# Kernel tuning notes

Hardware: AMD Instinct MI355X
Metric: run time of the kernel (lower is better)

The kernel has to match this reference:

```python
import jax, jax.numpy as jnp
import numpy as np

COMMITMENT_COST = 0.25
NUM_EMBEDDINGS = 4096
EMBEDDING_DIM = 256


def setup_inputs() -> dict:
    key = jax.random.key(0)
    k1, k2 = jax.random.split(key)
    inputs = jax.random.normal(k1, (32, EMBEDDING_DIM, 2048), dtype=jnp.float32)
    # nn.Embedding weight initialized uniform(-1/K, 1/K)
    codebook = jax.random.uniform(
        k2, (NUM_EMBEDDINGS, EMBEDDING_DIM), dtype=jnp.float32,
        minval=-1.0 / NUM_EMBEDDINGS, maxval=1.0 / NUM_EMBEDDINGS)
    return {"inputs": inputs, "codebook": codebook}


def reference(inputs, codebook):
    B, D, S = inputs.shape
    sg = jax.lax.stop_gradient
    # [B, D, S] -> [B*S, D]
    flat = jnp.transpose(inputs, (0, 2, 1)).reshape(-1, D)
    distances = (jnp.sum(flat ** 2, axis=1, keepdims=True)
                 + jnp.sum(codebook ** 2, axis=1)
                 - 2.0 * flat @ codebook.T)
    encoding_indices = jnp.argmin(distances, axis=1)  # [N]
    # direct gather (same math as one-hot @ codebook)
    quantized = codebook[encoding_indices].reshape(B, S, D)
    quantized = jnp.transpose(quantized, (0, 2, 1))  # [B, D, S]
    e_latent_loss = jnp.mean((sg(quantized) - inputs) ** 2)
    q_latent_loss = jnp.mean((quantized - sg(inputs)) ** 2)
    loss = COMMITMENT_COST * e_latent_loss + q_latent_loss
    # straight-through estimator
    quantized_st = inputs + sg(quantized - inputs)
    return quantized_st, loss
```

## Files before the change

### kernel.cpp

```cpp
#include <hip/hip_runtime.h>

#define K_CODES 4096
#define DIM 256
#define SEQ 2048
#define NTOK 65536

typedef __bf16 bf16x8 __attribute__((ext_vector_type(8)));
typedef float floatx4 __attribute__((ext_vector_type(4)));
typedef unsigned short u16x8 __attribute__((ext_vector_type(8)));

__device__ __forceinline__ unsigned short f2bf(float f) {
    union { float f; unsigned int u; } v; v.f = f;
    unsigned int u = v.u;
    unsigned int r = u + 0x7fffu + ((u >> 16) & 1u);
    return (unsigned short)(r >> 16);
}

__device__ __forceinline__ void async_cp16(const void* g, const void* lds_base) {
    typedef __attribute__((address_space(1))) const unsigned int guint;
    typedef __attribute__((address_space(3))) unsigned int luint;
    __builtin_amdgcn_global_load_lds(
        (guint*)(unsigned long long)g,
        (luint*)(unsigned int)(unsigned long long)lds_base,
        16, 0, 0);
}

__global__ __launch_bounds__(256) void k_prep(const float* __restrict__ cb,
        unsigned short* __restrict__ cb_swz, float* __restrict__ norms,
        float* __restrict__ loss_slot) {
    const int c = blockIdx.x;
    const int t = threadIdx.x;
    const int row_loc = t >> 3;
    const int ks = t & 7;
    const int row = c * 32 + row_loc;
    const float* src = cb + (size_t)row * DIM + ks * 32;
    float vals[32];
    float s = 0.0f;
    #pragma unroll
    for (int i = 0; i < 8; ++i) {
        floatx4 v = *(const floatx4*)(src + i * 4);
        #pragma unroll
        for (int j = 0; j < 4; ++j) { vals[i * 4 + j] = v[j]; s += v[j] * v[j]; }
    }
    const int ns = row_loc >> 4, col = row_loc & 15;
    #pragma unroll
    for (int quad = 0; quad < 4; ++quad) {
        u16x8 p;
        #pragma unroll
        for (int j = 0; j < 8; ++j) p[j] = f2bf(vals[quad * 8 + j]);
        *(u16x8*)(cb_swz + ((size_t)((c * 16 + ns * 8 + ks) * 64 + quad * 16 + col)) * 8) = p;
    }
    s += __shfl_xor(s, 1); s += __shfl_xor(s, 2); s += __shfl_xor(s, 4);
    if (ks == 0) norms[row] = s + 0.25f;
    if (c == 0 && t == 0) *loss_slot = 0.0f;
}

__global__ __launch_bounds__(256, 2) void k_argmin(const float* __restrict__ x,
        const unsigned short* __restrict__ cb_swz, const float* __restrict__ norms,
        unsigned int* __restrict__ halfmin, float* __restrict__ loss_slot) {
    __shared__ __align__(16) unsigned short xs[64 * 264];
    __shared__ __align__(16) unsigned short ring[2][8192];
    __shared__ float wpart[4];
    const int t = threadIdx.x;
    const int lane = t & 63, w = t >> 6;
    const int col = lane & 15, quad = lane >> 4;
    const int bx = blockIdx.x;
    const int h = bx & 1;
    const int tb = (bx >> 1) * 256;
    const int b = tb >> 11, s0 = tb & 2047;
    const float* xin = x + (size_t)b * DIM * SEQ;

    {
        const char* src = (const char*)cb_swz + (size_t)h * 64 * 16384;
        #pragma unroll
        for (int i = 0; i < 4; ++i)
            async_cp16(src + i * 4096 + w * 1024 + lane * 16,
                       (char*)ring[0] + i * 4096 + w * 1024);
    }

    bf16x8 af[4][8];
    float a2 = 0.0f;
    const int dg = t >> 4, sq = (t & 15) * 4;
    for (int ph = 0; ph < 4; ++ph) {
        const int sbase = s0 + ph * 64 + sq;
        for (int i = 0; i < 16; ++i) {
            int d = i * 16 + dg;
            floatx4 v = *(const floatx4*)(xin + (size_t)d * SEQ + sbase);
            a2 += v[0]*v[0] + v[1]*v[1] + v[2]*v[2] + v[3]*v[3];
            #pragma unroll
            for (int j = 0; j < 4; ++j) xs[(sq + j) * 264 + d] = f2bf(-2.0f * v[j]);
        }
        __syncthreads();
        if (w == ph) {
            #pragma unroll
            for (int m = 0; m < 4; ++m)
                #pragma unroll
                for (int ks = 0; ks < 8; ++ks)
                    af[m][ks] = *(const bf16x8*)&xs[(m * 16 + col) * 264
                                                    + quad * 8 + ks * 32];
        }
        __syncthreads();
    }
    #pragma unroll
    for (int off = 1; off < 64; off <<= 1) a2 += __shfl_xor(a2, off);
    if (lane == 0) wpart[w] = a2;
    __syncthreads();
    if (t == 0 && h == 0)
        atomicAdd(loss_slot,
                  (wpart[0] + wpart[1] + wpart[2] + wpart[3]) * (1.25f / 16777216.0f));

    unsigned int minkey[4][4];
    #pragma unroll
    for (int m = 0; m < 4; ++m)
        #pragma unroll
        for (int r = 0; r < 4; ++r) minkey[m][r] = 0xFFFFFFFFu;

    #pragma unroll 1
    for (int c = 0; c < 64; ++c) {
        __syncthreads();
        if (c < 63) {
            const char* src = (const char*)cb_swz + (size_t)(h * 64 + c + 1) * 16384;
            char* dst = (char*)ring[(c + 1) & 1];
            #pragma unroll
            for (int i = 0; i < 4; ++i)
                async_cp16(src + i * 4096 + w * 1024 + lane * 16,
                           dst + i * 4096 + w * 1024);
        }
        const unsigned short* buf = ring[c & 1];
        #pragma unroll
        for (int ns = 0; ns < 2; ++ns) {
            const float nv = norms[(h * 64 + c) * 32 + ns * 16 + col];
            bf16x8 bfrag[8];
            #pragma unroll
            for (int ks = 0; ks < 8; ++ks)
                bfrag[ks] = *(const bf16x8*)&buf[((ns * 8 + ks) * 64 + lane) * 8];
            floatx4 acc[4];
            #pragma unroll
            for (int m = 0; m < 4; ++m) acc[m] = (floatx4){nv, nv, nv, nv};
            #pragma unroll
            for (int ks = 0; ks < 8; ++ks)
                #pragma unroll
                for (int m = 0; m < 4; ++m)
                    acc[m] = __builtin_amdgcn_mfma_f32_16x16x32_bf16(
                                 af[m][ks], bfrag[ks], acc[m], 0, 0, 0);
            const unsigned int code = (unsigned int)((h * 64 + c) * 32 + ns * 16 + col);
            #pragma unroll
            for (int m = 0; m < 4; ++m)
                #pragma unroll
                for (int r = 0; r < 4; ++r) {
                    unsigned int key = (__float_as_uint(acc[m][r]) & 0xFFFFF000u) | code;
                    minkey[m][r] = key < minkey[m][r] ? key : minkey[m][r];
                }
        }
    }

    #pragma unroll
    for (int m = 0; m < 4; ++m)
        #pragma unroll
        for (int r = 0; r < 4; ++r) {
            unsigned int k = minkey[m][r];
            #pragma unroll
            for (int off = 8; off >= 1; off >>= 1) {
                unsigned int o = __shfl_xor(k, off);
                k = o < k ? o : k;
            }
            if (col == 0)
                halfmin[h * NTOK + tb + w * 64 + m * 16 + quad * 4 + r] = k;
        }
}

__global__ __launch_bounds__(256) void k_gather(const float* __restrict__ cb,
        const unsigned int* __restrict__ halfmin, float* __restrict__ out,
        float* __restrict__ loss_slot) {
    __shared__ int sidx[128];
    __shared__ float wp2[2];
    const int t = threadIdx.x;
    const int tb = blockIdx.x * 128;
    const int b = tb >> 11, s0 = tb & 2047;
    if (t < 128) {
        unsigned int k0 = halfmin[tb + t], k1 = halfmin[NTOK + tb + t];
        unsigned int km = k0 < k1 ? k0 : k1;
        sidx[t] = (int)(km & 0xFFFu);
        float dv = __uint_as_float(km & 0xFFFFF000u) - 0.25f;
        #pragma unroll
        for (int off = 1; off < 64; off <<= 1) dv += __shfl_xor(dv, off);
        if ((t & 63) == 0) wp2[t >> 6] = dv;
    }
    __syncthreads();
    if (t == 0) atomicAdd(loss_slot, (wp2[0] + wp2[1]) * (1.25f / 16777216.0f));
    const int q = t >> 3, dg = t & 7;
    int rows[4];
    #pragma unroll
    for (int k = 0; k < 4; ++k) rows[k] = sidx[q * 4 + k];
    float* ob = out + (size_t)b * DIM * SEQ + s0 + q * 4;
    #pragma unroll
    for (int i = 0; i < 8; ++i) {
        const int d0 = i * 32 + dg * 4;
        floatx4 v0 = *(const floatx4*)(cb + (size_t)rows[0] * DIM + d0);
        floatx4 v1 = *(const floatx4*)(cb + (size_t)rows[1] * DIM + d0);
        floatx4 v2 = *(const floatx4*)(cb + (size_t)rows[2] * DIM + d0);
        floatx4 v3 = *(const floatx4*)(cb + (size_t)rows[3] * DIM + d0);
        #pragma unroll
        for (int j = 0; j < 4; ++j) {
            floatx4 o = {v0[j], v1[j], v2[j], v3[j]};
            *(floatx4*)(ob + (size_t)(d0 + j) * SEQ) = o;
        }
    }
}

extern "C" void kernel_launch(void* const* d_in, const int* in_sizes, int n_in,
                              void* d_out, int out_size, void* d_ws, size_t ws_size,
                              hipStream_t stream) {
    const float* inputs   = (const float*)d_in[0];
    const float* codebook = (const float*)d_in[1];
    float* out = (float*)d_out;
    unsigned short* cb_swz = (unsigned short*)d_ws;
    float* norms = (float*)((char*)d_ws + (size_t)K_CODES * DIM * 2);
    unsigned int* halfmin = (unsigned int*)((char*)d_ws + (size_t)K_CODES * DIM * 2
                                            + K_CODES * 4);
    float* loss_slot = out + (out_size - 1);

    hipLaunchKernelGGL(k_prep,   dim3(K_CODES / 32),   dim3(256), 0, stream,
                       codebook, cb_swz, norms, loss_slot);
    hipLaunchKernelGGL(k_argmin, dim3(NTOK / 256 * 2), dim3(256), 0, stream,
                       inputs, cb_swz, norms, halfmin, loss_slot);
    hipLaunchKernelGGL(k_gather, dim3(NTOK / 128),     dim3(256), 0, stream,
                       codebook, halfmin, out, loss_slot);
}
```

Baseline: 239.9 us.

## Halve argmin token tile, alias x staging onto ring buffer, raise occupancy

The argmin kernel now handles 128 tokens per block instead of 256, so each wave holds two A-fragment sets instead of four. The separate padded x staging array is removed and its data is staged in the second ring buffer with an XOR swizzle in place of padding, which cuts LDS use. Launch bounds go from 2 to 3 blocks per SIMD and the grid doubles. The aim is more waves in flight to hide latency, at the cost of loading each codebook tile twice as often per token, which raises L2 traffic and lowers MFMA reuse per B fragment.

After: 257.7 us. 7.4% more time.

```diff
diff --git a/kernel.cpp b/kernel.cpp
--- a/kernel.cpp
+++ b/kernel.cpp
@@ -55,18 +55,18 @@
     if (c == 0 && t == 0) *loss_slot = 0.0f;
 }
 
-__global__ __launch_bounds__(256, 2) void k_argmin(const float* __restrict__ x,
+__global__ __launch_bounds__(256, 3) void k_argmin(const float* __restrict__ x,
         const unsigned short* __restrict__ cb_swz, const float* __restrict__ norms,
         unsigned int* __restrict__ halfmin, float* __restrict__ loss_slot) {
-    __shared__ __align__(16) unsigned short xs[64 * 264];
     __shared__ __align__(16) unsigned short ring[2][8192];
     __shared__ float wpart[4];
+    unsigned short* xs = ring[1];
     const int t = threadIdx.x;
     const int lane = t & 63, w = t >> 6;
     const int col = lane & 15, quad = lane >> 4;
     const int bx = blockIdx.x;
     const int h = bx & 1;
-    const int tb = (bx >> 1) * 256;
+    const int tb = (bx >> 1) * 128;
     const int b = tb >> 11, s0 = tb & 2047;
     const float* xin = x + (size_t)b * DIM * SEQ;
 
@@ -78,26 +78,31 @@
                        (char*)ring[0] + i * 4096 + w * 1024);
     }
 
-    bf16x8 af[4][8];
+    bf16x8 af0[8], af1[8];
     float a2 = 0.0f;
-    const int dg = t >> 4, sq = (t & 15) * 4;
-    for (int ph = 0; ph < 4; ++ph) {
-        const int sbase = s0 + ph * 64 + sq;
-        for (int i = 0; i < 16; ++i) {
-            int d = i * 16 + dg;
+    const int q = t & 7, dgp = t >> 3, sq = q * 4;
+    for (int p = 0; p < 4; ++p) {
+        const int sbase = s0 + p * 32 + sq;
+        #pragma unroll
+        for (int i = 0; i < 8; ++i) {
+            const int d = i * 32 + dgp;
             floatx4 v = *(const floatx4*)(xin + (size_t)d * SEQ + sbase);
             a2 += v[0]*v[0] + v[1]*v[1] + v[2]*v[2] + v[3]*v[3];
-            #pragma unroll
-            for (int j = 0; j < 4; ++j) xs[(sq + j) * 264 + d] = f2bf(-2.0f * v[j]);
+            const int chs = (d >> 3) ^ q;
+            #pragma unroll
+            for (int j = 0; j < 4; ++j)
+                xs[(sq + j) * 256 + chs * 8 + (d & 7)] = f2bf(-2.0f * v[j]);
         }
         __syncthreads();
-        if (w == ph) {
-            #pragma unroll
-            for (int m = 0; m < 4; ++m)
-                #pragma unroll
-                for (int ks = 0; ks < 8; ++ks)
-                    af[m][ks] = *(const bf16x8*)&xs[(m * 16 + col) * 264
-                                                    + quad * 8 + ks * 32];
+        if (w == p) {
+            #pragma unroll
+            for (int ks = 0; ks < 8; ++ks)
+                af0[ks] = *(const bf16x8*)
+                    &xs[col * 256 + (((quad + ks * 4) ^ (col >> 2)) * 8)];
+            #pragma unroll
+            for (int ks = 0; ks < 8; ++ks)
+                af1[ks] = *(const bf16x8*)
+                    &xs[(16 + col) * 256 + (((quad + ks * 4) ^ (4 + (col >> 2))) * 8)];
         }
         __syncthreads();
     }
@@ -109,11 +114,9 @@
         atomicAdd(loss_slot,
                   (wpart[0] + wpart[1] + wpart[2] + wpart[3]) * (1.25f / 16777216.0f));
 
-    unsigned int minkey[4][4];
-    #pragma unroll
-    for (int m = 0; m < 4; ++m)
-        #pragma unroll
-        for (int r = 0; r < 4; ++r) minkey[m][r] = 0xFFFFFFFFu;
+    unsigned int minkey0[4], minkey1[4];
+    #pragma unroll
+    for (int r = 0; r < 4; ++r) { minkey0[r] = 0xFFFFFFFFu; minkey1[r] = 0xFFFFFFFFu; }
 
     #pragma unroll 1
     for (int c = 0; c < 64; ++c) {
@@ -134,39 +137,45 @@
             #pragma unroll
             for (int ks = 0; ks < 8; ++ks)
                 bfrag[ks] = *(const bf16x8*)&buf[((ns * 8 + ks) * 64 + lane) * 8];
-            floatx4 acc[4];
-            #pragma unroll
-            for (int m = 0; m < 4; ++m) acc[m] = (floatx4){nv, nv, nv, nv};
-            #pragma unroll
-            for (int ks = 0; ks < 8; ++ks)
-                #pragma unroll
-                for (int m = 0; m < 4; ++m)
-                    acc[m] = __builtin_amdgcn_mfma_f32_16x16x32_bf16(
-                                 af[m][ks], bfrag[ks], acc[m], 0, 0, 0);
+            floatx4 acc0 = (floatx4){nv, nv, nv, nv};
+            floatx4 acc1 = (floatx4){nv, nv, nv, nv};
+            #pragma unroll
+            for (int ks = 0; ks < 8; ++ks) {
+                acc0 = __builtin_amdgcn_mfma_f32_16x16x32_bf16(
+                           af0[ks], bfrag[ks], acc0, 0, 0, 0);
+                acc1 = __builtin_amdgcn_mfma_f32_16x16x32_bf16(
+                           af1[ks], bfrag[ks], acc1, 0, 0, 0);
+            }
             const unsigned int code = (unsigned int)((h * 64 + c) * 32 + ns * 16 + col);
             #pragma unroll
-            for (int m = 0; m < 4; ++m)
-                #pragma unroll
-                for (int r = 0; r < 4; ++r) {
-                    unsigned int key = (__float_as_uint(acc[m][r]) & 0xFFFFF000u) | code;
-                    minkey[m][r] = key < minkey[m][r] ? key : minkey[m][r];
-                }
-        }
-    }
-
-    #pragma unroll
-    for (int m = 0; m < 4; ++m)
-        #pragma unroll
-        for (int r = 0; r < 4; ++r) {
-            unsigned int k = minkey[m][r];
-            #pragma unroll
-            for (int off = 8; off >= 1; off >>= 1) {
-                unsigned int o = __shfl_xor(k, off);
-                k = o < k ? o : k;
+            for (int r = 0; r < 4; ++r) {
+                unsigned int k0 = (__float_as_uint(acc0[r]) & 0xFFFFF000u) | code;
+                minkey0[r] = k0 < minkey0[r] ? k0 : minkey0[r];
+                unsigned int k1 = (__float_as_uint(acc1[r]) & 0xFFFFF000u) | code;
+                minkey1[r] = k1 < minkey1[r] ? k1 : minkey1[r];
             }
-            if (col == 0)
-                halfmin[h * NTOK + tb + w * 64 + m * 16 + quad * 4 + r] = k;
-        }
+        }
+    }
+
+    #pragma unroll
+    for (int r = 0; r < 4; ++r) {
+        unsigned int k = minkey0[r];
+        #pragma unroll
+        for (int off = 8; off >= 1; off >>= 1) {
+            unsigned int o = __shfl_xor(k, off);
+            k = o < k ? o : k;
+        }
+        if (col == 0)
+            halfmin[h * NTOK + tb + w * 32 + quad * 4 + r] = k;
+        unsigned int k2 = minkey1[r];
+        #pragma unroll
+        for (int off = 8; off >= 1; off >>= 1) {
+            unsigned int o = __shfl_xor(k2, off);
+            k2 = o < k2 ? o : k2;
+        }
+        if (col == 0)
+            halfmin[h * NTOK + tb + w * 32 + 16 + quad * 4 + r] = k2;
+    }
 }
 
 __global__ __launch_bounds__(256) void k_gather(const float* __restrict__ cb,
@@ -222,7 +231,7 @@
 
     hipLaunchKernelGGL(k_prep,   dim3(K_CODES / 32),   dim3(256), 0, stream,
                        codebook, cb_swz, norms, loss_slot);
-    hipLaunchKernelGGL(k_argmin, dim3(NTOK / 256 * 2), dim3(256), 0, stream,
+    hipLaunchKernelGGL(k_argmin, dim3(NTOK / 128 * 2), dim3(256), 0, stream,
                        inputs, cb_swz, norms, halfmin, loss_slot);
     hipLaunchKernelGGL(k_gather, dim3(NTOK / 128),     dim3(256), 0, stream,
                        codebook, halfmin, out, loss_slot);
```

## Double codebook chunk per stage, alias x staging into ring buffer with XOR swizzle

Applied to the files above, without the earlier changes.

The codebook pipeline now moves 64 codes (32 KB) per stage instead of 32, which halves the number of barrier-separated iterations. The x staging buffer reuses the second ring slot instead of its own padded array, with an XOR swizzle replacing the padding to avoid LDS bank conflicts. This keeps shared memory about the same while amortising sync and prefetch overhead. The cost is larger per-stage loads and less slack in prefetch timing.

Result: no change. 237.7 us (-0.9%).

```diff
diff --git a/kernel.cpp b/kernel.cpp
--- a/kernel.cpp
+++ b/kernel.cpp
@@ -58,9 +58,10 @@
 __global__ __launch_bounds__(256, 2) void k_argmin(const float* __restrict__ x,
         const unsigned short* __restrict__ cb_swz, const float* __restrict__ norms,
         unsigned int* __restrict__ halfmin, float* __restrict__ loss_slot) {
-    __shared__ __align__(16) unsigned short xs[64 * 264];
-    __shared__ __align__(16) unsigned short ring[2][8192];
+    __shared__ __align__(16) unsigned short ring0[16384];
+    __shared__ __align__(16) unsigned short ring1[16384];
     __shared__ float wpart[4];
+    unsigned short* xs = ring1;
     const int t = threadIdx.x;
     const int lane = t & 63, w = t >> 6;
     const int col = lane & 15, quad = lane >> 4;
@@ -71,33 +72,38 @@
     const float* xin = x + (size_t)b * DIM * SEQ;
 
     {
-        const char* src = (const char*)cb_swz + (size_t)h * 64 * 16384;
-        #pragma unroll
-        for (int i = 0; i < 4; ++i)
+        const char* src = (const char*)cb_swz + (size_t)h * 1048576;
+        #pragma unroll
+        for (int i = 0; i < 8; ++i)
             async_cp16(src + i * 4096 + w * 1024 + lane * 16,
-                       (char*)ring[0] + i * 4096 + w * 1024);
+                       (char*)ring0 + i * 4096 + w * 1024);
     }
 
     bf16x8 af[4][8];
     float a2 = 0.0f;
-    const int dg = t >> 4, sq = (t & 15) * 4;
+    const int dg = t >> 4, sq = (t & 15) * 4, key = t & 7;
     for (int ph = 0; ph < 4; ++ph) {
         const int sbase = s0 + ph * 64 + sq;
+        #pragma unroll
         for (int i = 0; i < 16; ++i) {
-            int d = i * 16 + dg;
+            const int d = i * 16 + dg;
             floatx4 v = *(const floatx4*)(xin + (size_t)d * SEQ + sbase);
             a2 += v[0]*v[0] + v[1]*v[1] + v[2]*v[2] + v[3]*v[3];
-            #pragma unroll
-            for (int j = 0; j < 4; ++j) xs[(sq + j) * 264 + d] = f2bf(-2.0f * v[j]);
+            const int chs = (d >> 3) ^ key;
+            #pragma unroll
+            for (int j = 0; j < 4; ++j)
+                xs[(sq + j) * 256 + chs * 8 + (d & 7)] = f2bf(-2.0f * v[j]);
         }
         __syncthreads();
         if (w == ph) {
             #pragma unroll
-            for (int m = 0; m < 4; ++m)
+            for (int m = 0; m < 4; ++m) {
+                const int rk = (m * 4 + (col >> 2)) & 7;
                 #pragma unroll
                 for (int ks = 0; ks < 8; ++ks)
-                    af[m][ks] = *(const bf16x8*)&xs[(m * 16 + col) * 264
-                                                    + quad * 8 + ks * 32];
+                    af[m][ks] = *(const bf16x8*)
+                        &xs[(m * 16 + col) * 256 + ((quad + ks * 4) ^ rk) * 8];
+            }
         }
         __syncthreads();
     }
@@ -116,20 +122,21 @@
         for (int r = 0; r < 4; ++r) minkey[m][r] = 0xFFFFFFFFu;
 
     #pragma unroll 1
-    for (int c = 0; c < 64; ++c) {
+    for (int cc = 0; cc < 32; ++cc) {
         __syncthreads();
-        if (c < 63) {
-            const char* src = (const char*)cb_swz + (size_t)(h * 64 + c + 1) * 16384;
-            char* dst = (char*)ring[(c + 1) & 1];
-            #pragma unroll
-            for (int i = 0; i < 4; ++i)
+        if (cc < 31) {
+            const char* src = (const char*)cb_swz + (size_t)h * 1048576
+                              + (size_t)(cc + 1) * 32768;
+            char* dst = (char*)(((cc + 1) & 1) ? ring1 : ring0);
+            #pragma unroll
+            for (int i = 0; i < 8; ++i)
                 async_cp16(src + i * 4096 + w * 1024 + lane * 16,
                            dst + i * 4096 + w * 1024);
         }
-        const unsigned short* buf = ring[c & 1];
-        #pragma unroll
-        for (int ns = 0; ns < 2; ++ns) {
-            const float nv = norms[(h * 64 + c) * 32 + ns * 16 + col];
+        const unsigned short* buf = (cc & 1) ? ring1 : ring0;
+        #pragma unroll
+        for (int ns = 0; ns < 4; ++ns) {
+            const float nv = norms[h * 2048 + cc * 64 + ns * 16 + col];
             bf16x8 bfrag[8];
             #pragma unroll
             for (int ks = 0; ks < 8; ++ks)
@@ -143,13 +150,13 @@
                 for (int m = 0; m < 4; ++m)
                     acc[m] = __builtin_amdgcn_mfma_f32_16x16x32_bf16(
                                  af[m][ks], bfrag[ks], acc[m], 0, 0, 0);
-            const unsigned int code = (unsigned int)((h * 64 + c) * 32 + ns * 16 + col);
+            const unsigned int code = (unsigned int)(h * 2048 + cc * 64 + ns * 16 + col);
             #pragma unroll
             for (int m = 0; m < 4; ++m)
                 #pragma unroll
                 for (int r = 0; r < 4; ++r) {
-                    unsigned int key = (__float_as_uint(acc[m][r]) & 0xFFFFF000u) | code;
-                    minkey[m][r] = key < minkey[m][r] ? key : minkey[m][r];
+                    unsigned int kk = (__float_as_uint(acc[m][r]) & 0xFFFFF000u) | code;
+                    minkey[m][r] = kk < minkey[m][r] ? kk : minkey[m][r];
                 }
         }
     }
```
